# Performance work log

Measured on AMD Instinct MI355X. Metric: run time of the kernel, lower is better.

The kernel has to match this reference:

```python
import jax, jax.numpy as jnp
import numpy as np

WS = 8          # window size
HEADS = 6
DIM = 192


def _rel_idx(ws):
    # index [q, k] -> flat relative-position index into table of size (2ws-1)^2
    pos = jnp.arange(ws * ws)
    ph, pw = pos // ws, pos % ws
    rel_h = ph[None, :] - ph[:, None] + ws - 1  # k_h - q_h + ws - 1
    rel_w = pw[None, :] - pw[:, None] + ws - 1
    return rel_h * (2 * ws - 1) + rel_w  # [ws*ws, ws*ws]


def setup_inputs() -> dict:
    key = jax.random.key(0)
    ks = jax.random.split(key, 4)
    x = jax.random.normal(ks[0], (4, DIM, 256, 256), jnp.float32)
    qkv_w = jax.random.normal(ks[1], (3 * DIM, DIM), jnp.float32) * 0.02  # 1x1 conv
    qkv_b = jnp.zeros((3 * DIM,), jnp.float32)
    out_w = jax.random.normal(ks[2], (DIM, DIM), jnp.float32) * 0.02      # 1x1 conv
    out_b = jnp.zeros((DIM,), jnp.float32)
    rpe_table = jax.random.normal(ks[3], (HEADS, (2 * WS - 1) ** 2), jnp.float32) * 0.001
    return {"x": x, "qkv_w": qkv_w, "qkv_b": qkv_b,
            "out_w": out_w, "out_b": out_b, "rpe_table": rpe_table}


def reference(x, qkv_w, qkv_b, out_w, out_b, rpe_table):
    B, C, H, W = x.shape
    ws, heads = WS, HEADS
    hd, wd = H // ws, W // ws          # H,W chosen divisible by ws -> pad is no-op
    c = C // heads                     # head dim
    n = ws * ws                        # tokens per window

    # 1x1 conv to qkv
    qkv = jnp.einsum('bchw,oc->bohw', x, qkv_w) + qkv_b[None, :, None, None]
    # feat_to_win: b (3 heads c) (hd ws) (wd ws) -> 3, (b hd wd), heads, n, c
    qkv = qkv.reshape(B, 3, heads, c, hd, ws, wd, ws)
    qkv = qkv.transpose(1, 0, 4, 6, 2, 5, 7, 3).reshape(3, B * hd * wd, heads, n, c)
    q, k, v = qkv[0], qkv[1], qkv[2]

    bias = rpe_table[:, _rel_idx(ws)]  # [heads, n, n]
    scale = c ** -0.5
    scores = jnp.einsum('whqc,whkc->whqk', q, k) * scale + bias[None]
    attn = jax.nn.softmax(scores, axis=-1)
    out = jnp.einsum('whqk,whkc->whqc', attn, v)

    # win_to_feat: (b hd wd) heads n c -> b (heads c) H W
    out = out.reshape(B, hd, wd, heads, ws, ws, c)
    out = out.transpose(0, 3, 6, 1, 4, 2, 5).reshape(B, C, H, W)

    out = jnp.einsum('bchw,oc->bohw', out, out_w) + out_b[None, :, None, None]
    return out
```

## Files before the change

### kernel.cpp

```cpp
#include <hip/hip_runtime.h>
#include <cstdint>
#include <cstddef>

typedef __attribute__((ext_vector_type(8))) short short8;
typedef __attribute__((ext_vector_type(4))) float floatx4;
typedef __attribute__((ext_vector_type(16))) float floatx16;

#define SEG 50331648ull

__device__ __forceinline__ unsigned short bf16rne(float f) {
  union { float f; unsigned int u; } c; c.f = f;
  unsigned int u = c.u;
  return (unsigned short)((u + 0x7fffu + ((u >> 16) & 1u)) >> 16);
}
__device__ __forceinline__ unsigned int packbf(float a, float b) {
  return (unsigned int)bf16rne(a) | ((unsigned int)bf16rne(b) << 16);
}
__device__ __forceinline__ unsigned int cvtpk(float lo, float hi) {
  unsigned int r;
  asm("v_cvt_pk_bf16_f32 %0, %1, %2" : "=v"(r) : "v"(lo), "v"(hi));
  return r;
}

__global__ __launch_bounds__(256) void w_prep(
    const float* __restrict__ wq, const float* __restrict__ qb,
    const float* __restrict__ ow,
    unsigned short* __restrict__ wqb, unsigned short* __restrict__ owb,
    float* __restrict__ qbs) {
  const float S = 0.17677669529663687f;
  int id = blockIdx.x * 256 + threadIdx.x;
  if (id < 55296) {
    float s = (id < 18432) ? S : 1.0f;
    ((unsigned int*)wqb)[id] = packbf(wq[2 * id] * s, wq[2 * id + 1] * s);
  } else if (id < 55296 + 18432) {
    int j = id - 55296;
    ((unsigned int*)owb)[j] = packbf(ow[2 * j], ow[2 * j + 1]);
  } else if (id < 55296 + 18432 + 576) {
    int j = id - 55296 - 18432;
    qbs[j] = qb[j] * (j < 192 ? S : 1.0f);
  }
}

__global__ void bias_prep(const float* __restrict__ rpe, float* __restrict__ bias_d) {
  const int head = blockIdx.x;
  const int tid = threadIdx.x;
  for (int e = tid; e < 4096; e += 256) {
    int f = e >> 10;
    int lane = (e >> 4) & 63;
    int reg = e & 15;
    int kt2 = f >> 1, qt2 = f & 1;
    int qq = qt2 * 32 + (lane & 31);
    int kk = kt2 * 32 + (reg & 3) + 8 * (reg >> 2) + 4 * (lane >> 5);
    int idx = ((kk >> 3) - (qq >> 3) + 7) * 15 + ((kk & 7) - (qq & 7) + 7);
    bias_d[((size_t)(head * 4 + f) * 64 + lane) * 16 + reg] = rpe[head * 225 + idx];
  }
}

__global__ __launch_bounds__(256) void x_to_bf16(const float* __restrict__ x,
                                                 unsigned short* __restrict__ xb) {
  __shared__ float Tl[64][65];
  const int tid = threadIdx.x;
  const int ptile = blockIdx.x, cc = blockIdx.y, b = blockIdx.z;
  const float* src = x + ((size_t)(b * 192 + cc * 64)) * 65536 + ptile * 64;
  {
    int row = tid >> 2;
    int cb = (tid & 3) * 4;
#pragma unroll
    for (int rr = 0; rr < 4; ++rr) {
      int col = cb + rr * 16;
      float4 v = *(const float4*)(src + (size_t)row * 65536 + col);
      *(float4*)&Tl[row][col] = v;
    }
  }
  __syncthreads();
  unsigned short* dst = xb + ((size_t)b * 65536 + (size_t)ptile * 64) * 192 + cc * 64;
  {
    int p_l = tid >> 2;
    int c0 = (tid & 3) * 16;
    unsigned int w[8];
#pragma unroll
    for (int e = 0; e < 8; ++e)
      w[e] = cvtpk(Tl[c0 + 2 * e][p_l], Tl[c0 + 2 * e + 1][p_l]);
    *(uint4*)(dst + (size_t)p_l * 192 + c0)     = make_uint4(w[0], w[1], w[2], w[3]);
    *(uint4*)(dst + (size_t)p_l * 192 + c0 + 8) = make_uint4(w[4], w[5], w[6], w[7]);
  }
}

#define WP 200
#define XP 200
__global__ __launch_bounds__(256) void qkv_mm(
    const unsigned short* __restrict__ xb, const unsigned short* __restrict__ wqb,
    const float* __restrict__ qbs,
    unsigned short* __restrict__ q, unsigned short* __restrict__ k,
    unsigned short* __restrict__ v) {
  __shared__ unsigned short Xl[128 * XP];
  __shared__ unsigned short Wl[64 * WP];
  const int tid = threadIdx.x;
  const int pt = blockIdx.x, b = blockIdx.y;
  const int lane = tid & 63, w = tid >> 6;
  const int n16 = lane & 15, quad = lane >> 4;

  const unsigned short* xrow = xb + ((size_t)b * 65536 + (size_t)pt * 128) * 192;
#pragma unroll
  for (int r = 0; r < 12; ++r) {
    int c = tid + 256 * r;
    int row = c / 24;
    int col = (c - row * 24) * 8;
    short8 xv = *(const short8*)(xrow + (size_t)c * 8);
    *(short8*)&Xl[row * XP + col] = xv;
  }
  int wrow[6], wcol[6];
#pragma unroll
  for (int r = 0; r < 6; ++r) {
    int id = tid + 256 * r;
    wrow[r] = id / 24;
    wcol[r] = (id - wrow[r] * 24) * 8;
  }
  short8 wpre[6];
#pragma unroll
  for (int r = 0; r < 6; ++r)
    wpre[r] = *(const short8*)(wqb + (size_t)wrow[r] * 192 + wcol[r]);
#pragma unroll
  for (int r = 0; r < 6; ++r)
    *(short8*)&Wl[wrow[r] * WP + wcol[r]] = wpre[r];
  __syncthreads();

  const floatx4 fz = {0.f, 0.f, 0.f, 0.f};
#pragma unroll 1
  for (int ot = 0; ot < 9; ++ot) {
    if (ot < 8) {
      const unsigned short* wn = wqb + (size_t)(ot + 1) * 64 * 192;
#pragma unroll
      for (int r = 0; r < 6; ++r)
        wpre[r] = *(const short8*)(wn + (size_t)wrow[r] * 192 + wcol[r]);
    }
    floatx4 acc[4][2];
#pragma unroll
    for (int i = 0; i < 4; ++i)
#pragma unroll
      for (int j = 0; j < 2; ++j) acc[i][j] = fz;
#pragma unroll
    for (int k0 = 0; k0 < 192; k0 += 32) {
      short8 a[4], bf[2];
#pragma unroll
      for (int i = 0; i < 4; ++i)
        a[i] = *(const short8*)&Wl[(16 * i + n16) * WP + k0 + quad * 8];
#pragma unroll
      for (int j = 0; j < 2; ++j)
        bf[j] = *(const short8*)&Xl[(w * 32 + 16 * j + n16) * XP + k0 + quad * 8];
#pragma unroll
      for (int i = 0; i < 4; ++i)
#pragma unroll
        for (int j = 0; j < 2; ++j)
          acc[i][j] = __builtin_amdgcn_mfma_f32_16x16x32_bf16(a[i], bf[j], acc[i][j], 0, 0, 0);
    }
    __syncthreads();
    if (ot < 8) {
#pragma unroll
      for (int r = 0; r < 6; ++r)
        *(short8*)&Wl[wrow[r] * WP + wcol[r]] = wpre[r];
    }
    __syncthreads();

    const int sel = ot / 3;
    unsigned short* dst = (sel == 0) ? q : ((sel == 1) ? k : v);
    const int h = pt >> 1;
    float4 bb[4];
#pragma unroll
    for (int i = 0; i < 4; ++i)
      bb[i] = *(const float4*)(qbs + ot * 64 + 16 * i + quad * 4);
#pragma unroll
    for (int j = 0; j < 2; ++j) {
      int wcol2 = w * 32 + 16 * j + n16;
      int wc = ((pt & 1) << 7) + wcol2;
      int win = (b << 10) + (h >> 3) * 32 + (wc >> 3);
      int t = ((h & 7) << 3) + (wc & 7);
#pragma unroll
      for (int i = 0; i < 4; ++i) {
        int og = ot * 64 + 16 * i + quad * 4;
        int off = og - sel * 192;
        int head = off >> 5, c = off & 31;
        *(uint2*)(dst + ((size_t)(win * 6 + head) * 64 + t) * 32 + c) =
            make_uint2(cvtpk(acc[i][j][0] + bb[i].x, acc[i][j][1] + bb[i].y),
                       cvtpk(acc[i][j][2] + bb[i].z, acc[i][j][3] + bb[i].w));
      }
    }
  }
}

__global__ __launch_bounds__(256) void attn(
    const unsigned short* __restrict__ q, const unsigned short* __restrict__ k,
    const unsigned short* __restrict__ v, const float* __restrict__ bias_d,
    unsigned short* __restrict__ AO) {
  __shared__ unsigned short vl[4][32 * 72];
  const int tid = threadIdx.x, w = tid >> 6, lane = tid & 63;
  const int m32 = lane & 31, half = lane >> 5;
  const int wh = blockIdx.x * 4 + w;
  const int win = wh / 6, head = wh - win * 6;
  const unsigned short* qb = q + (size_t)wh * 2048;
  const unsigned short* kb = k + (size_t)wh * 2048;
  const unsigned short* vb = v + (size_t)wh * 2048;

  short8 vrow[4];
#pragma unroll
  for (int c8 = 0; c8 < 4; ++c8)
    vrow[c8] = *(const short8*)(vb + lane * 32 + c8 * 8);

  short8 ka[2][2];
#pragma unroll
  for (int kt2 = 0; kt2 < 2; ++kt2)
#pragma unroll
    for (int cc = 0; cc < 2; ++cc)
      ka[kt2][cc] = *(const short8*)(kb + (size_t)(kt2 * 32 + m32) * 32 + cc * 16 + half * 8);

  unsigned short* vlw = (unsigned short*)vl[w];
#pragma unroll
  for (int c8 = 0; c8 < 4; ++c8)
#pragma unroll
    for (int e = 0; e < 8; ++e)
      vlw[(c8 * 8 + e) * 72 + lane] = (unsigned short)vrow[c8][e];

  short8 va[4];
#pragma unroll
  for (int k16 = 0; k16 < 4; ++k16)
    va[k16] = *(const short8*)&vlw[m32 * 72 + k16 * 16 + half * 8];

  const float* bD = bias_d + (size_t)head * 4096;
  const floatx16 fz16 = {0.f,0.f,0.f,0.f,0.f,0.f,0.f,0.f,0.f,0.f,0.f,0.f,0.f,0.f,0.f,0.f};

#pragma unroll
  for (int qt2 = 0; qt2 < 2; ++qt2) {
    float4 bb[8];
#pragma unroll
    for (int g = 0; g < 4; ++g)
      bb[g] = *(const float4*)(bD + ((size_t)(qt2 * 64) + lane) * 16 + g * 4);
#pragma unroll
    for (int g = 0; g < 4; ++g)
      bb[4 + g] = *(const float4*)(bD + ((size_t)((2 + qt2) * 64) + lane) * 16 + g * 4);

    short8 qf0 = *(const short8*)(qb + (size_t)(qt2 * 32 + m32) * 32 + half * 8);
    short8 qf1 = *(const short8*)(qb + (size_t)(qt2 * 32 + m32) * 32 + 16 + half * 8);

    floatx16 st0 = __builtin_amdgcn_mfma_f32_32x32x16_bf16(ka[0][0], qf0, fz16, 0, 0, 0);
    st0 = __builtin_amdgcn_mfma_f32_32x32x16_bf16(ka[0][1], qf1, st0, 0, 0, 0);
    floatx16 st1 = __builtin_amdgcn_mfma_f32_32x32x16_bf16(ka[1][0], qf0, fz16, 0, 0, 0);
    st1 = __builtin_amdgcn_mfma_f32_32x32x16_bf16(ka[1][1], qf1, st1, 0, 0, 0);

    float x[32];
#pragma unroll
    for (int r = 0; r < 16; ++r) x[r]      = st0[r] + ((const float*)&bb[r >> 2])[r & 3];
#pragma unroll
    for (int r = 0; r < 16; ++r) x[16 + r] = st1[r] + ((const float*)&bb[4 + (r >> 2)])[r & 3];

    float mx = x[0];
#pragma unroll
    for (int r = 1; r < 32; ++r) mx = fmaxf(mx, x[r]);
    mx = fmaxf(mx, __shfl_xor(mx, 32));
    float s = 0.f;
#pragma unroll
    for (int r = 0; r < 32; ++r) { x[r] = __expf(x[r] - mx); s += x[r]; }
    s += __shfl_xor(s, 32);
    float iv = 1.0f / s;

    unsigned int u[16];
#pragma unroll
    for (int j = 0; j < 16; ++j) u[j] = cvtpk(x[2 * j], x[2 * j + 1]);

    floatx16 o = fz16;
#pragma unroll
    for (int k16 = 0; k16 < 4; ++k16) {
      int base = (k16 >> 1) * 8 + (k16 & 1) * 4;
      unsigned int a0 = u[base + 0], b0 = u[base + 2];
      unsigned int a1 = u[base + 1], b1 = u[base + 3];
      asm("v_permlane32_swap_b32 %0, %1" : "+v"(a0), "+v"(b0));
      asm("v_permlane32_swap_b32 %0, %1" : "+v"(a1), "+v"(b1));
      union { unsigned int wd[4]; short8 s8; } bw;
      bw.wd[0] = a0; bw.wd[1] = a1; bw.wd[2] = b0; bw.wd[3] = b1;
      o = __builtin_amdgcn_mfma_f32_32x32x16_bf16(va[k16], bw.s8, o, 0, 0, 0);
    }

    const int t = qt2 * 32 + m32;
    const int bimg = win >> 10, rem = win & 1023;
    const int h0 = (rem >> 5) << 3, w0 = (rem & 31) << 3;
    const size_t pix = ((size_t)bimg << 16) + (size_t)(h0 + (t >> 3)) * 256 + w0 + (t & 7);
    unsigned short* dstp = AO + pix * 192 + head * 32 + half * 4;
#pragma unroll
    for (int g = 0; g < 4; ++g) {
      float v0 = o[4 * g + 0] * iv, v1 = o[4 * g + 1] * iv;
      float v2 = o[4 * g + 2] * iv, v3 = o[4 * g + 3] * iv;
      *(uint2*)(dstp + g * 8) = make_uint2(cvtpk(v0, v1), cvtpk(v2, v3));
    }
  }
}

__global__ __launch_bounds__(256) void out_mm(
    const unsigned short* __restrict__ AO, const unsigned short* __restrict__ owb,
    const float* __restrict__ b2, float* __restrict__ out) {
  __shared__ unsigned short Xl[128 * XP];
  __shared__ unsigned short Wl[64 * WP];
  const int tid = threadIdx.x;
  const int pt = blockIdx.x, b = blockIdx.y;
  const int lane = tid & 63, w = tid >> 6;
  const int n16 = lane & 15, quad = lane >> 4;

  const unsigned short* arow = AO + ((size_t)b * 65536 + (size_t)pt * 128) * 192;
#pragma unroll
  for (int r = 0; r < 12; ++r) {
    int c = tid + 256 * r;
    int row = c / 24;
    int col = (c - row * 24) * 8;
    short8 xv = *(const short8*)(arow + (size_t)c * 8);
    *(short8*)&Xl[row * XP + col] = xv;
  }
  int wrow[6], wcol[6];
#pragma unroll
  for (int r = 0; r < 6; ++r) {
    int id = tid + 256 * r;
    wrow[r] = id / 24;
    wcol[r] = (id - wrow[r] * 24) * 8;
  }
  short8 wpre[6];
#pragma unroll
  for (int r = 0; r < 6; ++r)
    wpre[r] = *(const short8*)(owb + (size_t)wrow[r] * 192 + wcol[r]);
#pragma unroll
  for (int r = 0; r < 6; ++r)
    *(short8*)&Wl[wrow[r] * WP + wcol[r]] = wpre[r];
  __syncthreads();

  const floatx4 fz = {0.f, 0.f, 0.f, 0.f};
#pragma unroll 1
  for (int ot = 0; ot < 3; ++ot) {
    if (ot < 2) {
      const unsigned short* wn = owb + (size_t)(ot + 1) * 64 * 192;
#pragma unroll
      for (int r = 0; r < 6; ++r)
        wpre[r] = *(const short8*)(wn + (size_t)wrow[r] * 192 + wcol[r]);
    }
    floatx4 acc[2][4];
#pragma unroll
    for (int i = 0; i < 2; ++i)
#pragma unroll
      for (int j = 0; j < 4; ++j) acc[i][j] = fz;
#pragma unroll
    for (int k0 = 0; k0 < 192; k0 += 32) {
      short8 a[2], bf[4];
#pragma unroll
      for (int i = 0; i < 2; ++i)
        a[i] = *(const short8*)&Xl[(w * 32 + 16 * i + n16) * XP + k0 + quad * 8];
#pragma unroll
      for (int j = 0; j < 4; ++j)
        bf[j] = *(const short8*)&Wl[(16 * j + n16) * WP + k0 + quad * 8];
#pragma unroll
      for (int i = 0; i < 2; ++i)
#pragma unroll
        for (int j = 0; j < 4; ++j)
          acc[i][j] = __builtin_amdgcn_mfma_f32_16x16x32_bf16(a[i], bf[j], acc[i][j], 0, 0, 0);
    }
    __syncthreads();
    if (ot < 2) {
#pragma unroll
      for (int r = 0; r < 6; ++r)
        *(short8*)&Wl[wrow[r] * WP + wcol[r]] = wpre[r];
    }
    __syncthreads();

#pragma unroll
    for (int j = 0; j < 4; ++j) {
      int o = ot * 64 + 16 * j + n16;
      float bj = b2[o];
      float* obase = out + ((size_t)b * 192 + o) * 65536 + (size_t)pt * 128;
#pragma unroll
      for (int i = 0; i < 2; ++i) {
        int p = w * 32 + 16 * i + quad * 4;
        *(float4*)(obase + p) = make_float4(acc[i][j][0] + bj, acc[i][j][1] + bj,
                                            acc[i][j][2] + bj, acc[i][j][3] + bj);
      }
    }
  }
}

extern "C" void kernel_launch(void* const* d_in, const int* in_sizes, int n_in,
                              void* d_out, int out_size, void* d_ws, size_t ws_size,
                              hipStream_t stream) {
  const float* x     = (const float*)d_in[0];
  const float* qkv_w = (const float*)d_in[1];
  const float* qkv_b = (const float*)d_in[2];
  const float* out_w = (const float*)d_in[3];
  const float* out_b = (const float*)d_in[4];
  const float* rpe   = (const float*)d_in[5];
  float* out = (float*)d_out;

  unsigned short* xb = (unsigned short*)d_ws;
  unsigned short* AO = xb;
  unsigned short* q  = xb + SEG;
  unsigned short* k  = q + SEG;
  unsigned short* v  = k + SEG;
  unsigned short* wqb = v + SEG;
  unsigned short* owb = wqb + 110592;
  float* qbs = (float*)(owb + 36864);
  float* bias_d = qbs + 576;

  w_prep<<<291, 256, 0, stream>>>(qkv_w, qkv_b, out_w, wqb, owb, qbs);
  bias_prep<<<6, 256, 0, stream>>>(rpe, bias_d);
  x_to_bf16<<<dim3(1024, 3, 4), 256, 0, stream>>>(x, xb);
  qkv_mm<<<dim3(512, 4), 256, 0, stream>>>(xb, wqb, qbs, q, k, v);
  attn<<<6144, 256, 0, stream>>>(q, k, v, bias_d, AO);
  out_mm<<<dim3(512, 4), 256, 0, stream>>>(AO, owb, out_b, out);
}
```

Measured before the change: 645.9 us.

## Process four windows per wave with per-head bias staged in LDS

The attention kernel now assigns one head per block and has each wave loop over four windows. The head's relative-position bias is loaded once into shared memory and reused, replacing the per-window global bias reads. The launch shrinks to a quarter of the blocks. Max and sum reductions become tree-shaped to shorten dependency chains. The trade-off is fewer blocks in flight and less latency hiding, since the per-window loads are now serialized inside each wave.

```diff
diff --git a/kernel.cpp b/kernel.cpp
--- a/kernel.cpp
+++ b/kernel.cpp
@@ -193,102 +193,129 @@
     const unsigned short* __restrict__ v, const float* __restrict__ bias_d,
     unsigned short* __restrict__ AO) {
   __shared__ unsigned short vl[4][32 * 72];
+  __shared__ float4 bl[16 * 64];
   const int tid = threadIdx.x, w = tid >> 6, lane = tid & 63;
   const int m32 = lane & 31, half = lane >> 5;
-  const int wh = blockIdx.x * 4 + w;
-  const int win = wh / 6, head = wh - win * 6;
-  const unsigned short* qb = q + (size_t)wh * 2048;
-  const unsigned short* kb = k + (size_t)wh * 2048;
-  const unsigned short* vb = v + (size_t)wh * 2048;
-
-  short8 vrow[4];
-#pragma unroll
-  for (int c8 = 0; c8 < 4; ++c8)
-    vrow[c8] = *(const short8*)(vb + lane * 32 + c8 * 8);
-
-  short8 ka[2][2];
-#pragma unroll
-  for (int kt2 = 0; kt2 < 2; ++kt2)
-#pragma unroll
-    for (int cc = 0; cc < 2; ++cc)
-      ka[kt2][cc] = *(const short8*)(kb + (size_t)(kt2 * 32 + m32) * 32 + cc * 16 + half * 8);
+  const int head = blockIdx.x >> 8;
+  const int gw = blockIdx.x * 4 + w;
+  const int win0 = (gw & 1023) << 2;
+
+  {
+    const float4* src = (const float4*)(bias_d + (size_t)head * 4096);
+    for (int s = tid; s < 1024; s += 256) {
+      int f = s >> 8, ln = (s >> 2) & 63, g = s & 3;
+      bl[(f * 4 + g) * 64 + ln] = src[s];
+    }
+  }
+  __syncthreads();
 
   unsigned short* vlw = (unsigned short*)vl[w];
-#pragma unroll
-  for (int c8 = 0; c8 < 4; ++c8)
-#pragma unroll
-    for (int e = 0; e < 8; ++e)
-      vlw[(c8 * 8 + e) * 72 + lane] = (unsigned short)vrow[c8][e];
-
-  short8 va[4];
-#pragma unroll
-  for (int k16 = 0; k16 < 4; ++k16)
-    va[k16] = *(const short8*)&vlw[m32 * 72 + k16 * 16 + half * 8];
-
-  const float* bD = bias_d + (size_t)head * 4096;
   const floatx16 fz16 = {0.f,0.f,0.f,0.f,0.f,0.f,0.f,0.f,0.f,0.f,0.f,0.f,0.f,0.f,0.f,0.f};
 
 #pragma unroll
-  for (int qt2 = 0; qt2 < 2; ++qt2) {
-    float4 bb[8];
-#pragma unroll
-    for (int g = 0; g < 4; ++g)
-      bb[g] = *(const float4*)(bD + ((size_t)(qt2 * 64) + lane) * 16 + g * 4);
-#pragma unroll
-    for (int g = 0; g < 4; ++g)
-      bb[4 + g] = *(const float4*)(bD + ((size_t)((2 + qt2) * 64) + lane) * 16 + g * 4);
-
-    short8 qf0 = *(const short8*)(qb + (size_t)(qt2 * 32 + m32) * 32 + half * 8);
-    short8 qf1 = *(const short8*)(qb + (size_t)(qt2 * 32 + m32) * 32 + 16 + half * 8);
-
-    floatx16 st0 = __builtin_amdgcn_mfma_f32_32x32x16_bf16(ka[0][0], qf0, fz16, 0, 0, 0);
-    st0 = __builtin_amdgcn_mfma_f32_32x32x16_bf16(ka[0][1], qf1, st0, 0, 0, 0);
-    floatx16 st1 = __builtin_amdgcn_mfma_f32_32x32x16_bf16(ka[1][0], qf0, fz16, 0, 0, 0);
-    st1 = __builtin_amdgcn_mfma_f32_32x32x16_bf16(ka[1][1], qf1, st1, 0, 0, 0);
-
-    float x[32];
-#pragma unroll
-    for (int r = 0; r < 16; ++r) x[r]      = st0[r] + ((const float*)&bb[r >> 2])[r & 3];
-#pragma unroll
-    for (int r = 0; r < 16; ++r) x[16 + r] = st1[r] + ((const float*)&bb[4 + (r >> 2)])[r & 3];
-
-    float mx = x[0];
-#pragma unroll
-    for (int r = 1; r < 32; ++r) mx = fmaxf(mx, x[r]);
-    mx = fmaxf(mx, __shfl_xor(mx, 32));
-    float s = 0.f;
-#pragma unroll
-    for (int r = 0; r < 32; ++r) { x[r] = __expf(x[r] - mx); s += x[r]; }
-    s += __shfl_xor(s, 32);
-    float iv = 1.0f / s;
-
-    unsigned int u[16];
-#pragma unroll
-    for (int j = 0; j < 16; ++j) u[j] = cvtpk(x[2 * j], x[2 * j + 1]);
-
-    floatx16 o = fz16;
-#pragma unroll
-    for (int k16 = 0; k16 < 4; ++k16) {
-      int base = (k16 >> 1) * 8 + (k16 & 1) * 4;
-      unsigned int a0 = u[base + 0], b0 = u[base + 2];
-      unsigned int a1 = u[base + 1], b1 = u[base + 3];
-      asm("v_permlane32_swap_b32 %0, %1" : "+v"(a0), "+v"(b0));
-      asm("v_permlane32_swap_b32 %0, %1" : "+v"(a1), "+v"(b1));
-      union { unsigned int wd[4]; short8 s8; } bw;
-      bw.wd[0] = a0; bw.wd[1] = a1; bw.wd[2] = b0; bw.wd[3] = b1;
-      o = __builtin_amdgcn_mfma_f32_32x32x16_bf16(va[k16], bw.s8, o, 0, 0, 0);
-    }
-
-    const int t = qt2 * 32 + m32;
-    const int bimg = win >> 10, rem = win & 1023;
-    const int h0 = (rem >> 5) << 3, w0 = (rem & 31) << 3;
-    const size_t pix = ((size_t)bimg << 16) + (size_t)(h0 + (t >> 3)) * 256 + w0 + (t & 7);
-    unsigned short* dstp = AO + pix * 192 + head * 32 + half * 4;
-#pragma unroll
-    for (int g = 0; g < 4; ++g) {
-      float v0 = o[4 * g + 0] * iv, v1 = o[4 * g + 1] * iv;
-      float v2 = o[4 * g + 2] * iv, v3 = o[4 * g + 3] * iv;
-      *(uint2*)(dstp + g * 8) = make_uint2(cvtpk(v0, v1), cvtpk(v2, v3));
+  for (int wi = 0; wi < 4; ++wi) {
+    const int win = win0 + wi;
+    const size_t base = ((size_t)win * 6 + head) * 2048;
+    const unsigned short* qb = q + base;
+    const unsigned short* kb = k + base;
+    const unsigned short* vb = v + base;
+
+    short8 vrow[4];
+#pragma unroll
+    for (int c8 = 0; c8 < 4; ++c8)
+      vrow[c8] = *(const short8*)(vb + lane * 32 + c8 * 8);
+
+    short8 ka[2][2];
+#pragma unroll
+    for (int kt2 = 0; kt2 < 2; ++kt2)
+#pragma unroll
+      for (int cc = 0; cc < 2; ++cc)
+        ka[kt2][cc] = *(const short8*)(kb + (size_t)(kt2 * 32 + m32) * 32 + cc * 16 + half * 8);
+
+#pragma unroll
+    for (int c8 = 0; c8 < 4; ++c8)
+#pragma unroll
+      for (int e = 0; e < 8; ++e)
+        vlw[(c8 * 8 + e) * 72 + lane] = (unsigned short)vrow[c8][e];
+
+    short8 va[4];
+#pragma unroll
+    for (int k16 = 0; k16 < 4; ++k16)
+      va[k16] = *(const short8*)&vlw[m32 * 72 + k16 * 16 + half * 8];
+
+#pragma unroll
+    for (int qt2 = 0; qt2 < 2; ++qt2) {
+      float4 bb[8];
+#pragma unroll
+      for (int g = 0; g < 4; ++g) bb[g] = bl[(qt2 * 4 + g) * 64 + lane];
+#pragma unroll
+      for (int g = 0; g < 4; ++g) bb[4 + g] = bl[((2 + qt2) * 4 + g) * 64 + lane];
+
+      short8 qf0 = *(const short8*)(qb + (size_t)(qt2 * 32 + m32) * 32 + half * 8);
+      short8 qf1 = *(const short8*)(qb + (size_t)(qt2 * 32 + m32) * 32 + 16 + half * 8);
+
+      floatx16 st0 = __builtin_amdgcn_mfma_f32_32x32x16_bf16(ka[0][0], qf0, fz16, 0, 0, 0);
+      st0 = __builtin_amdgcn_mfma_f32_32x32x16_bf16(ka[0][1], qf1, st0, 0, 0, 0);
+      floatx16 st1 = __builtin_amdgcn_mfma_f32_32x32x16_bf16(ka[1][0], qf0, fz16, 0, 0, 0);
+      st1 = __builtin_amdgcn_mfma_f32_32x32x16_bf16(ka[1][1], qf1, st1, 0, 0, 0);
+
+      float x[32];
+#pragma unroll
+      for (int r = 0; r < 16; ++r) x[r]      = st0[r] + ((const float*)&bb[r >> 2])[r & 3];
+#pragma unroll
+      for (int r = 0; r < 16; ++r) x[16 + r] = st1[r] + ((const float*)&bb[4 + (r >> 2)])[r & 3];
+
+      float t16[16];
+#pragma unroll
+      for (int r = 0; r < 16; ++r) t16[r] = fmaxf(x[r], x[r + 16]);
+#pragma unroll
+      for (int r = 0; r < 8; ++r) t16[r] = fmaxf(t16[r], t16[r + 8]);
+#pragma unroll
+      for (int r = 0; r < 4; ++r) t16[r] = fmaxf(t16[r], t16[r + 4]);
+      float mx = fmaxf(fmaxf(t16[0], t16[1]), fmaxf(t16[2], t16[3]));
+      mx = fmaxf(mx, __shfl_xor(mx, 32));
+
+#pragma unroll
+      for (int r = 0; r < 32; ++r) x[r] = __expf(x[r] - mx);
+      float s16[16];
+#pragma unroll
+      for (int r = 0; r < 16; ++r) s16[r] = x[r] + x[r + 16];
+#pragma unroll
+      for (int r = 0; r < 8; ++r) s16[r] += s16[r + 8];
+#pragma unroll
+      for (int r = 0; r < 4; ++r) s16[r] += s16[r + 4];
+      float s = (s16[0] + s16[1]) + (s16[2] + s16[3]);
+      s += __shfl_xor(s, 32);
+      float iv = 1.0f / s;
+
+      unsigned int u[16];
+#pragma unroll
+      for (int j = 0; j < 16; ++j) u[j] = cvtpk(x[2 * j], x[2 * j + 1]);
+
+      floatx16 o = fz16;
+#pragma unroll
+      for (int k16 = 0; k16 < 4; ++k16) {
+        int ub = (k16 >> 1) * 8 + (k16 & 1) * 4;
+        unsigned int a0 = u[ub + 0], b0 = u[ub + 2];
+        unsigned int a1 = u[ub + 1], b1 = u[ub + 3];
+        asm("v_permlane32_swap_b32 %0, %1" : "+v"(a0), "+v"(b0));
+        asm("v_permlane32_swap_b32 %0, %1" : "+v"(a1), "+v"(b1));
+        union { unsigned int wd[4]; short8 s8; } bw;
+        bw.wd[0] = a0; bw.wd[1] = a1; bw.wd[2] = b0; bw.wd[3] = b1;
+        o = __builtin_amdgcn_mfma_f32_32x32x16_bf16(va[k16], bw.s8, o, 0, 0, 0);
+      }
+
+      const int t = qt2 * 32 + m32;
+      const int bimg = win >> 10, rem = win & 1023;
+      const int h0 = (rem >> 5) << 3, w0 = (rem & 31) << 3;
+      const size_t pix = ((size_t)bimg << 16) + (size_t)(h0 + (t >> 3)) * 256 + w0 + (t & 7);
+      unsigned short* dstp = AO + pix * 192 + head * 32 + half * 4;
+#pragma unroll
+      for (int g = 0; g < 4; ++g) {
+        float v0 = o[4 * g + 0] * iv, v1 = o[4 * g + 1] * iv;
+        float v2 = o[4 * g + 2] * iv, v3 = o[4 * g + 3] * iv;
+        *(uint2*)(dstp + g * 8) = make_uint2(cvtpk(v0, v1), cvtpk(v2, v3));
+      }
     }
   }
 }
@@ -405,6 +432,6 @@
   bias_prep<<<6, 256, 0, stream>>>(rpe, bias_d);
   x_to_bf16<<<dim3(1024, 3, 4), 256, 0, stream>>>(x, xb);
   qkv_mm<<<dim3(512, 4), 256, 0, stream>>>(xb, wqb, qbs, q, k, v);
-  attn<<<6144, 256, 0, stream>>>(q, k, v, bias_d, AO);
+  attn<<<1536, 256, 0, stream>>>(q, k, v, bias_d, AO);
   out_mm<<<dim3(512, 4), 256, 0, stream>>>(AO, owb, out_b, out);
 }
```

Measured after the change: 651.5 us. No clear change (+0.9%).
